# Kernel optimization log

Hardware: AMD Instinct MI355X
Metric: run time of the kernel (lower is better)

## Reference

```python
import jax, jax.numpy as jnp
import numpy as np

CE_WEIGHT = 1.0
TRIPLET_WEIGHT = 0.1
MARGIN = 0.2


def setup_inputs() -> dict:
    key = jax.random.key(0)
    k1, k2, k3 = jax.random.split(key, 3)
    B, D, V = 4096, 512, 6000
    logits = jax.random.normal(k1, (B, V), dtype=jnp.float32)
    embeddings = jax.random.normal(k2, (B, D), dtype=jnp.float32)
    labels = jax.random.randint(k3, (B,), 0, 512, dtype=jnp.int64)
    return {"logits": logits, "embeddings": embeddings, "labels": labels}


def _pairwise_dist(emb):
    # Euclidean cdist via gram matrix; safe sqrt (zero grad where d2 == 0).
    sq = jnp.sum(emb * emb, axis=-1)  # [B]
    d2 = sq[:, None] + sq[None, :] - 2.0 * (emb @ emb.T)  # [B, B]
    d2 = jnp.maximum(d2, 0.0)
    safe = jnp.where(d2 > 0.0, d2, 1.0)
    return jnp.where(d2 > 0.0, jnp.sqrt(safe), 0.0)


def _losses(logits, embeddings, labels):
    B = logits.shape[0]
    # Cross entropy (mean reduction, matching nn.CrossEntropyLoss).
    logp = jax.nn.log_softmax(logits, axis=-1)
    ce_loss = -jnp.mean(jnp.take_along_axis(logp, labels[:, None], axis=1)[:, 0])

    # Batch-hard triplet loss, fully vectorized (one masked amax/amin per row).
    dist = _pairwise_dist(embeddings)  # [B, B]
    same = labels[:, None] == labels[None, :]  # [B, B]
    eye = jnp.eye(B, dtype=bool)
    pos_mask = same & ~eye
    neg_mask = ~same
    neg_inf = jnp.float32(-np.inf)
    pos_inf = jnp.float32(np.inf)
    hardest_pos = jnp.max(jnp.where(pos_mask, dist, neg_inf), axis=1)  # [B]
    hardest_neg = jnp.min(jnp.where(neg_mask, dist, pos_inf), axis=1)  # [B]
    valid = jnp.any(pos_mask, axis=1) & jnp.any(neg_mask, axis=1)  # [B]
    per_row = jax.nn.relu(hardest_pos - hardest_neg + MARGIN)
    per_row = jnp.where(valid, per_row, 0.0)
    n_valid = jnp.sum(valid.astype(jnp.float32))
    triplet_loss = jnp.where(n_valid > 0, jnp.sum(per_row) / jnp.maximum(n_valid, 1.0), 0.0)

    total_loss = CE_WEIGHT * ce_loss + TRIPLET_WEIGHT * triplet_loss
    return total_loss, ce_loss, triplet_loss


def reference(logits, embeddings, labels):
    return _losses(logits, embeddings, labels)
```

## Files before the change

### kernel.cpp

```cpp
#include <hip/hip_runtime.h>
#include <hip/hip_bf16.h>
#include <math.h>

#define BN   4096
#define DN   512
#define VN   6000
#define NCLS 512

typedef __attribute__((ext_vector_type(8)))  short short8;
typedef __attribute__((ext_vector_type(16))) float f32x16;

__device__ __forceinline__ unsigned short f2bf(float x) {
  unsigned int u = __float_as_uint(x);
  u = (u + 0x7FFFu + ((u >> 16) & 1u)) >> 16;
  return (unsigned short)u;
}

__device__ __forceinline__ void gld_lds16(const unsigned short* g, unsigned short* l) {
  __builtin_amdgcn_global_load_lds(
      (const __attribute__((address_space(1))) void*)g,
      (__attribute__((address_space(3))) void*)l, 16, 0, 0);
}

__launch_bounds__(256)
__global__ void prep_kernel(const float* __restrict__ emb, const int* __restrict__ labels,
                            unsigned short* __restrict__ embh, float* __restrict__ sqn,
                            int* __restrict__ cnt, int* __restrict__ posb,
                            int* __restrict__ negb) {
  const int row  = blockIdx.x * 4 + (threadIdx.x >> 6);
  const int lane = threadIdx.x & 63;
  const float4* rp = (const float4*)(emb + (size_t)row * DN);
  float4 a = rp[lane];
  float4 b = rp[lane + 64];
  float ss = a.x * a.x + a.y * a.y + a.z * a.z + a.w * a.w
           + b.x * b.x + b.y * b.y + b.z * b.z + b.w * b.w;
  ushort4 ha, hb;
  ha.x = f2bf(a.x); ha.y = f2bf(a.y); ha.z = f2bf(a.z); ha.w = f2bf(a.w);
  hb.x = f2bf(b.x); hb.y = f2bf(b.y); hb.z = f2bf(b.z); hb.w = f2bf(b.w);
  ushort4* wp = (ushort4*)(embh + (size_t)row * DN);
  wp[lane] = ha;
  wp[lane + 64] = hb;
#pragma unroll
  for (int off = 1; off < 64; off <<= 1) ss += __shfl_xor(ss, off);
  if (lane == 0) {
    sqn[row] = ss;
    posb[row] = 0;
    negb[row] = 0x7F800000;
    atomicAdd(cnt + labels[row], 1);
  }
}

__device__ __forceinline__ void triplet_job(int t, unsigned short* sA, unsigned short* sB,
                                            const unsigned short* __restrict__ embh,
                                            const float* __restrict__ sqn,
                                            const int* __restrict__ labels,
                                            int* __restrict__ posb,
                                            int* __restrict__ negb, int lane) {
  const int m = lane & 31;
  const int half = lane >> 5;

  int J = (int)((sqrtf(8.f * (float)t + 1.f) - 1.f) * 0.5f);
  while ((J + 1) * (J + 2) / 2 <= t) ++J;
  while (J * (J + 1) / 2 > t) --J;
  const int I = t - J * (J + 1) / 2;
  const int i0 = I * 64, j0 = J * 64;
  const bool diag = (I == J);

  const int lrow = lane >> 3;
  const int lchk = (lane & 7) ^ lrow;
  const unsigned short* gA = embh + (size_t)(i0 + lrow) * DN + lchk * 8;
  const unsigned short* gB = embh + (size_t)(j0 + lrow) * DN + lchk * 8;

  f32x16 acc[2][2] = {};
  f32x16 accT[2][2] = {};

  for (int ks = 0; ks < 8; ++ks) {
    const int kk = ks * 64;
    asm volatile("s_waitcnt lgkmcnt(0)" ::: "memory");
#pragma unroll
    for (int s = 0; s < 8; ++s)
      gld_lds16(gA + kk + (size_t)s * 8 * DN, &sA[s * 8 * 64]);
#pragma unroll
    for (int s = 0; s < 8; ++s)
      gld_lds16(gB + kk + (size_t)s * 8 * DN, &sB[s * 8 * 64]);
    asm volatile("s_waitcnt vmcnt(0)" ::: "memory");
#pragma unroll
    for (int q = 0; q < 4; ++q) {
      const int c = q * 2 + half;
      const int sw = ((c ^ (m & 7)) * 8);
      short8 a0 = *(const short8*)&sA[m * 64 + sw];
      short8 a1 = *(const short8*)&sA[(32 + m) * 64 + sw];
      short8 b0 = *(const short8*)&sB[m * 64 + sw];
      short8 b1 = *(const short8*)&sB[(32 + m) * 64 + sw];
      acc[0][0]  = __builtin_amdgcn_mfma_f32_32x32x16_bf16(a0, b0, acc[0][0], 0, 0, 0);
      acc[0][1]  = __builtin_amdgcn_mfma_f32_32x32x16_bf16(a0, b1, acc[0][1], 0, 0, 0);
      acc[1][0]  = __builtin_amdgcn_mfma_f32_32x32x16_bf16(a1, b0, acc[1][0], 0, 0, 0);
      acc[1][1]  = __builtin_amdgcn_mfma_f32_32x32x16_bf16(a1, b1, acc[1][1], 0, 0, 0);
      accT[0][0] = __builtin_amdgcn_mfma_f32_32x32x16_bf16(b0, a0, accT[0][0], 0, 0, 0);
      accT[0][1] = __builtin_amdgcn_mfma_f32_32x32x16_bf16(b0, a1, accT[0][1], 0, 0, 0);
      accT[1][0] = __builtin_amdgcn_mfma_f32_32x32x16_bf16(b1, a0, accT[1][0], 0, 0, 0);
      accT[1][1] = __builtin_amdgcn_mfma_f32_32x32x16_bf16(b1, a1, accT[1][1], 0, 0, 0);
    }
  }

  {
    const int gj0 = j0 + m, gj1 = j0 + 32 + m;
    const int cl0 = labels[gj0], cl1 = labels[gj1];
    const float cq0 = sqn[gj0], cq1 = sqn[gj1];
    float p0 = 0.f, p1 = 0.f, n0 = INFINITY, n1 = INFINITY;
#pragma unroll
    for (int rb = 0; rb < 2; ++rb) {
#pragma unroll
      for (int r = 0; r < 16; ++r) {
        const int gi = i0 + rb * 32 + (r & 3) + 8 * (r >> 2) + 4 * half;
        const int rl = labels[gi];
        const float rq = sqn[gi];
        const float d0 = fmaf(-2.f, acc[rb][0][r], rq + cq0);
        const float d1 = fmaf(-2.f, acc[rb][1][r], rq + cq1);
        if (rl == cl0) { if (gi != gj0) p0 = fmaxf(p0, d0); } else n0 = fminf(n0, d0);
        if (rl == cl1) { if (gi != gj1) p1 = fmaxf(p1, d1); } else n1 = fminf(n1, d1);
      }
    }
    p0 = fmaxf(p0, __shfl_xor(p0, 32)); n0 = fminf(n0, __shfl_xor(n0, 32));
    p1 = fmaxf(p1, __shfl_xor(p1, 32)); n1 = fminf(n1, __shfl_xor(n1, 32));
    if (half == 0) {
      atomicMax(posb + gj0, __float_as_int(p0));
      atomicMin(negb + gj0, __float_as_int(n0));
      atomicMax(posb + gj1, __float_as_int(p1));
      atomicMin(negb + gj1, __float_as_int(n1));
    }
  }

  if (!diag) {
    const int gj0 = i0 + m, gj1 = i0 + 32 + m;
    const int cl0 = labels[gj0], cl1 = labels[gj1];
    const float cq0 = sqn[gj0], cq1 = sqn[gj1];
    float p0 = 0.f, p1 = 0.f, n0 = INFINITY, n1 = INFINITY;
#pragma unroll
    for (int rb = 0; rb < 2; ++rb) {
#pragma unroll
      for (int r = 0; r < 16; ++r) {
        const int gi = j0 + rb * 32 + (r & 3) + 8 * (r >> 2) + 4 * half;
        const int rl = labels[gi];
        const float rq = sqn[gi];
        const float d0 = fmaf(-2.f, accT[rb][0][r], rq + cq0);
        const float d1 = fmaf(-2.f, accT[rb][1][r], rq + cq1);
        if (rl == cl0) p0 = fmaxf(p0, d0); else n0 = fminf(n0, d0);
        if (rl == cl1) p1 = fmaxf(p1, d1); else n1 = fminf(n1, d1);
      }
    }
    p0 = fmaxf(p0, __shfl_xor(p0, 32)); n0 = fminf(n0, __shfl_xor(n0, 32));
    p1 = fmaxf(p1, __shfl_xor(p1, 32)); n1 = fminf(n1, __shfl_xor(n1, 32));
    if (half == 0) {
      atomicMax(posb + gj0, __float_as_int(p0));
      atomicMin(negb + gj0, __float_as_int(n0));
      atomicMax(posb + gj1, __float_as_int(p1));
      atomicMin(negb + gj1, __float_as_int(n1));
    }
  }
}

__launch_bounds__(64, 2)
__global__ void fused_kernel(const float* __restrict__ logits,
                             const int* __restrict__ labels,
                             float* __restrict__ ce_part,
                             const unsigned short* __restrict__ embh,
                             const float* __restrict__ sqn,
                             int* __restrict__ posb, int* __restrict__ negb) {
  __shared__ unsigned short smem[8192];
  const int b = blockIdx.x;
  const int lane = threadIdx.x;

  int trip_job, ce_row;
  if (b < 32) {
    trip_job = 2048 + b; ce_row = -1;
  } else {
    const int g = (b - 32) / 3, r = (b - 32) % 3;
    if (r == 0) { trip_job = g; ce_row = -1; }
    else        { trip_job = -1; ce_row = g * 2 + (r - 1); }
  }

  if (trip_job >= 0) {
    triplet_job(trip_job, smem, smem + 4096, embh, sqn, labels, posb, negb, lane);
    return;
  }

  const float* rp = logits + (size_t)ce_row * VN;
  const float xlab = rp[labels[ce_row]];
  const float4* q = (const float4*)rp;
  float4 v[24];
#pragma unroll
  for (int u = 0; u < 23; ++u) v[u] = q[lane + u * 64];
  if (lane < 28) v[23] = q[lane + 23 * 64];
  float s = 0.f;
#pragma unroll
  for (int u = 0; u < 23; ++u)
    s += __expf(v[u].x) + __expf(v[u].y) + __expf(v[u].z) + __expf(v[u].w);
  if (lane < 28)
    s += __expf(v[23].x) + __expf(v[23].y) + __expf(v[23].z) + __expf(v[23].w);
#pragma unroll
  for (int off = 1; off < 64; off <<= 1) s += __shfl_xor(s, off);
  if (lane == 0) ce_part[ce_row] = logf(s) - xlab;
}

__launch_bounds__(1024)
__global__ void finalize_kernel(const int* __restrict__ posb, const int* __restrict__ negb,
                                const int* __restrict__ labels, const int* __restrict__ cnt,
                                const float* __restrict__ ce_part, float* __restrict__ out) {
  const int tid = threadIdx.x;
  float cesum = 0.f, sum = 0.f, nv = 0.f;
#pragma unroll
  for (int u = 0; u < 4; ++u) {
    const int i = tid + u * 1024;
    cesum += ce_part[i];
    int c = cnt[labels[i]];
    float p = sqrtf(fmaxf(__int_as_float(posb[i]), 0.f));
    float n = sqrtf(fmaxf(__int_as_float(negb[i]), 0.f));
    float t = fmaxf(p - n + 0.2f, 0.f);
    if (c >= 2 && c < BN) { sum += t; nv += 1.f; }
  }
#pragma unroll
  for (int off = 1; off < 64; off <<= 1) {
    cesum += __shfl_xor(cesum, off);
    sum   += __shfl_xor(sum, off);
    nv    += __shfl_xor(nv, off);
  }
  __shared__ float s0[16], s1[16], s2[16];
  if ((tid & 63) == 0) { s0[tid >> 6] = cesum; s1[tid >> 6] = sum; s2[tid >> 6] = nv; }
  __syncthreads();
  if (tid == 0) {
    cesum = 0.f; sum = 0.f; nv = 0.f;
#pragma unroll
    for (int wv = 0; wv < 16; ++wv) { cesum += s0[wv]; sum += s1[wv]; nv += s2[wv]; }
    float trip = (nv > 0.f) ? sum / nv : 0.f;
    float ce = cesum * (1.f / BN);
    out[0] = ce + 0.1f * trip;
    out[1] = ce;
    out[2] = trip;
  }
}

extern "C" void kernel_launch(void* const* d_in, const int* in_sizes, int n_in,
                              void* d_out, int out_size, void* d_ws, size_t ws_size,
                              hipStream_t stream) {
  const float* logits = (const float*)d_in[0];
  const float* emb    = (const float*)d_in[1];
  const int*   labels = (const int*)d_in[2];
  float* out = (float*)d_out;

  char* ws = (char*)d_ws;
  unsigned short* embh = (unsigned short*)ws;
  float* sqn    = (float*)(ws + (size_t)BN * DN * 2);
  int*   posb   = (int*)((char*)sqn  + (size_t)BN * 4);
  int*   negb   = (int*)((char*)posb + (size_t)BN * 4);
  int*   cnt    = (int*)((char*)negb + (size_t)BN * 4);
  float* ce_part = (float*)((char*)cnt + (size_t)NCLS * 4);

  hipMemsetAsync(cnt, 0, (size_t)NCLS * 4, stream);
  hipLaunchKernelGGL(prep_kernel, dim3(BN / 4), dim3(256), 0, stream,
                     emb, labels, embh, sqn, cnt, posb, negb);
  hipLaunchKernelGGL(fused_kernel, dim3(32 + 2048 * 3), dim3(64), 0, stream,
                     logits, labels, ce_part, embh, sqn, posb, negb);
  hipLaunchKernelGGL(finalize_kernel, dim3(1), dim3(1024), 0, stream,
                     posb, negb, labels, cnt, ce_part, out);
}
```

Before: 182.0 us.

## Split fused triplet/CE kernel into separate triplet and cross-entropy kernels

Replaces the single interleaved kernel, which mixed triplet GEMM jobs with per-row cross-entropy blocks, with two sequential launches: a triplet kernel of 2080 single-wave blocks and a CE kernel that processes four rows per 256-thread block. This removes the per-block job dispatch and lets each kernel get its own occupancy and launch bounds. In exchange it gives up overlapping the memory-bound CE reduction with the compute-bound triplet work and adds one extra launch.

```diff
diff --git a/kernel.cpp b/kernel.cpp
--- a/kernel.cpp
+++ b/kernel.cpp
@@ -161,32 +161,23 @@
 }
 
 __launch_bounds__(64, 2)
-__global__ void fused_kernel(const float* __restrict__ logits,
-                             const int* __restrict__ labels,
-                             float* __restrict__ ce_part,
-                             const unsigned short* __restrict__ embh,
-                             const float* __restrict__ sqn,
-                             int* __restrict__ posb, int* __restrict__ negb) {
+__global__ void trip_kernel(const unsigned short* __restrict__ embh,
+                            const float* __restrict__ sqn,
+                            const int* __restrict__ labels,
+                            int* __restrict__ posb, int* __restrict__ negb) {
   __shared__ unsigned short smem[8192];
-  const int b = blockIdx.x;
-  const int lane = threadIdx.x;
-
-  int trip_job, ce_row;
-  if (b < 32) {
-    trip_job = 2048 + b; ce_row = -1;
-  } else {
-    const int g = (b - 32) / 3, r = (b - 32) % 3;
-    if (r == 0) { trip_job = g; ce_row = -1; }
-    else        { trip_job = -1; ce_row = g * 2 + (r - 1); }
-  }
-
-  if (trip_job >= 0) {
-    triplet_job(trip_job, smem, smem + 4096, embh, sqn, labels, posb, negb, lane);
-    return;
-  }
-
-  const float* rp = logits + (size_t)ce_row * VN;
-  const float xlab = rp[labels[ce_row]];
+  triplet_job(blockIdx.x, smem, smem + 4096, embh, sqn, labels, posb, negb,
+              threadIdx.x);
+}
+
+__launch_bounds__(256, 4)
+__global__ void ce_kernel(const float* __restrict__ logits,
+                          const int* __restrict__ labels,
+                          float* __restrict__ ce_part) {
+  const int row  = blockIdx.x * 4 + (threadIdx.x >> 6);
+  const int lane = threadIdx.x & 63;
+  const float* rp = logits + (size_t)row * VN;
+  const float xlab = rp[labels[row]];
   const float4* q = (const float4*)rp;
   float4 v[24];
 #pragma unroll
@@ -200,7 +191,7 @@
     s += __expf(v[23].x) + __expf(v[23].y) + __expf(v[23].z) + __expf(v[23].w);
 #pragma unroll
   for (int off = 1; off < 64; off <<= 1) s += __shfl_xor(s, off);
-  if (lane == 0) ce_part[ce_row] = logf(s) - xlab;
+  if (lane == 0) ce_part[row] = logf(s) - xlab;
 }
 
 __launch_bounds__(1024)
@@ -259,8 +250,10 @@
   hipMemsetAsync(cnt, 0, (size_t)NCLS * 4, stream);
   hipLaunchKernelGGL(prep_kernel, dim3(BN / 4), dim3(256), 0, stream,
                      emb, labels, embh, sqn, cnt, posb, negb);
-  hipLaunchKernelGGL(fused_kernel, dim3(32 + 2048 * 3), dim3(64), 0, stream,
-                     logits, labels, ce_part, embh, sqn, posb, negb);
+  hipLaunchKernelGGL(trip_kernel, dim3(2080), dim3(64), 0, stream,
+                     embh, sqn, labels, posb, negb);
+  hipLaunchKernelGGL(ce_kernel, dim3(BN / 4), dim3(256), 0, stream,
+                     logits, labels, ce_part);
   hipLaunchKernelGGL(finalize_kernel, dim3(1), dim3(1024), 0, stream,
                      posb, negb, labels, cnt, ce_part, out);
 }
```

Measured after the change: 191.7 us. 5.4% more time.

## Drop transposed MFMA accumulators; derive row-side reductions via cross-lane shuffles

Applied to the files above, without the earlier changes.

Off-diagonal tiles of the symmetric Gram matrix used to run a second set of MFMAs (accT) to produce the transposed tile. That set is removed, and the row-side hardest pos/neg values are now reduced from the same acc registers with 5-step butterfly shuffles across the 32 columns, followed by per-row atomics. This halves MFMA work and frees 64 accumulator VGPRs, which is why launch bounds rise to 3 waves per SIMD. In exchange it adds many shuffles and about twice as many atomics per tile.

```diff
diff --git a/kernel.cpp b/kernel.cpp
--- a/kernel.cpp
+++ b/kernel.cpp
@@ -72,7 +72,6 @@
   const unsigned short* gB = embh + (size_t)(j0 + lrow) * DN + lchk * 8;
 
   f32x16 acc[2][2] = {};
-  f32x16 accT[2][2] = {};
 
   for (int ks = 0; ks < 8; ++ks) {
     const int kk = ks * 64;
@@ -92,14 +91,10 @@
       short8 a1 = *(const short8*)&sA[(32 + m) * 64 + sw];
       short8 b0 = *(const short8*)&sB[m * 64 + sw];
       short8 b1 = *(const short8*)&sB[(32 + m) * 64 + sw];
-      acc[0][0]  = __builtin_amdgcn_mfma_f32_32x32x16_bf16(a0, b0, acc[0][0], 0, 0, 0);
-      acc[0][1]  = __builtin_amdgcn_mfma_f32_32x32x16_bf16(a0, b1, acc[0][1], 0, 0, 0);
-      acc[1][0]  = __builtin_amdgcn_mfma_f32_32x32x16_bf16(a1, b0, acc[1][0], 0, 0, 0);
-      acc[1][1]  = __builtin_amdgcn_mfma_f32_32x32x16_bf16(a1, b1, acc[1][1], 0, 0, 0);
-      accT[0][0] = __builtin_amdgcn_mfma_f32_32x32x16_bf16(b0, a0, accT[0][0], 0, 0, 0);
-      accT[0][1] = __builtin_amdgcn_mfma_f32_32x32x16_bf16(b0, a1, accT[0][1], 0, 0, 0);
-      accT[1][0] = __builtin_amdgcn_mfma_f32_32x32x16_bf16(b1, a0, accT[1][0], 0, 0, 0);
-      accT[1][1] = __builtin_amdgcn_mfma_f32_32x32x16_bf16(b1, a1, accT[1][1], 0, 0, 0);
+      acc[0][0] = __builtin_amdgcn_mfma_f32_32x32x16_bf16(a0, b0, acc[0][0], 0, 0, 0);
+      acc[0][1] = __builtin_amdgcn_mfma_f32_32x32x16_bf16(a0, b1, acc[0][1], 0, 0, 0);
+      acc[1][0] = __builtin_amdgcn_mfma_f32_32x32x16_bf16(a1, b0, acc[1][0], 0, 0, 0);
+      acc[1][1] = __builtin_amdgcn_mfma_f32_32x32x16_bf16(a1, b1, acc[1][1], 0, 0, 0);
     }
   }
 
@@ -119,6 +114,20 @@
         const float d1 = fmaf(-2.f, acc[rb][1][r], rq + cq1);
         if (rl == cl0) { if (gi != gj0) p0 = fmaxf(p0, d0); } else n0 = fminf(n0, d0);
         if (rl == cl1) { if (gi != gj1) p1 = fmaxf(p1, d1); } else n1 = fminf(n1, d1);
+        if (!diag) {
+          float pi = 0.f, ni = INFINITY;
+          if (rl == cl0) pi = d0; else ni = d0;
+          if (rl == cl1) pi = fmaxf(pi, d1); else ni = fminf(ni, d1);
+#pragma unroll
+          for (int off = 1; off < 32; off <<= 1) {
+            pi = fmaxf(pi, __shfl_xor(pi, off));
+            ni = fminf(ni, __shfl_xor(ni, off));
+          }
+          if (m == 0) {
+            atomicMax(posb + gi, __float_as_int(pi));
+            atomicMin(negb + gi, __float_as_int(ni));
+          }
+        }
       }
     }
     p0 = fmaxf(p0, __shfl_xor(p0, 32)); n0 = fminf(n0, __shfl_xor(n0, 32));
@@ -130,37 +139,9 @@
       atomicMin(negb + gj1, __float_as_int(n1));
     }
   }
-
-  if (!diag) {
-    const int gj0 = i0 + m, gj1 = i0 + 32 + m;
-    const int cl0 = labels[gj0], cl1 = labels[gj1];
-    const float cq0 = sqn[gj0], cq1 = sqn[gj1];
-    float p0 = 0.f, p1 = 0.f, n0 = INFINITY, n1 = INFINITY;
-#pragma unroll
-    for (int rb = 0; rb < 2; ++rb) {
-#pragma unroll
-      for (int r = 0; r < 16; ++r) {
-        const int gi = j0 + rb * 32 + (r & 3) + 8 * (r >> 2) + 4 * half;
-        const int rl = labels[gi];
-        const float rq = sqn[gi];
-        const float d0 = fmaf(-2.f, accT[rb][0][r], rq + cq0);
-        const float d1 = fmaf(-2.f, accT[rb][1][r], rq + cq1);
-        if (rl == cl0) p0 = fmaxf(p0, d0); else n0 = fminf(n0, d0);
-        if (rl == cl1) p1 = fmaxf(p1, d1); else n1 = fminf(n1, d1);
-      }
-    }
-    p0 = fmaxf(p0, __shfl_xor(p0, 32)); n0 = fminf(n0, __shfl_xor(n0, 32));
-    p1 = fmaxf(p1, __shfl_xor(p1, 32)); n1 = fminf(n1, __shfl_xor(n1, 32));
-    if (half == 0) {
-      atomicMax(posb + gj0, __float_as_int(p0));
-      atomicMin(negb + gj0, __float_as_int(n0));
-      atomicMax(posb + gj1, __float_as_int(p1));
-      atomicMin(negb + gj1, __float_as_int(n1));
-    }
-  }
-}
-
-__launch_bounds__(64, 2)
+}
+
+__launch_bounds__(64, 3)
 __global__ void fused_kernel(const float* __restrict__ logits,
                              const int* __restrict__ labels,
                              float* __restrict__ ce_part,
```

Measured after the change: 194.1 us. 6.7% more time.

## Double-buffer triplet GEMM LDS tiles and stage labels/norms in LDS

Applied to the files above, without the earlier changes.

The triplet tile loop now double-buffers its LDS tiles. The next K-slice is prefetched with global_load_lds while MFMAs run on the current slice, using a partial vmcnt wait in place of a full drain each step. Per-row labels and squared norms are loaded once per lane and staged in shared memory for the epilogue, replacing many scattered global loads. Shared memory per block doubles to 32KB, which may reduce occupancy alongside the other per-block state.

```diff
diff --git a/kernel.cpp b/kernel.cpp
--- a/kernel.cpp
+++ b/kernel.cpp
@@ -50,7 +50,7 @@
   }
 }
 
-__device__ __forceinline__ void triplet_job(int t, unsigned short* sA, unsigned short* sB,
+__device__ __forceinline__ void triplet_job(int t, unsigned short* smem,
                                             const unsigned short* __restrict__ embh,
                                             const float* __restrict__ sqn,
                                             const int* __restrict__ labels,
@@ -66,6 +66,11 @@
   const int i0 = I * 64, j0 = J * 64;
   const bool diag = (I == J);
 
+  const int   li = labels[i0 + lane];
+  const float qi = sqn[i0 + lane];
+  const int   lj = labels[j0 + lane];
+  const float qj = sqn[j0 + lane];
+
   const int lrow = lane >> 3;
   const int lchk = (lane & 7) ^ lrow;
   const unsigned short* gA = embh + (size_t)(i0 + lrow) * DN + lchk * 8;
@@ -74,16 +79,29 @@
   f32x16 acc[2][2] = {};
   f32x16 accT[2][2] = {};
 
+#pragma unroll
+  for (int s = 0; s < 8; ++s) {
+    gld_lds16(gA + (size_t)s * 8 * DN, smem + s * 512);
+    gld_lds16(gB + (size_t)s * 8 * DN, smem + 4096 + s * 512);
+  }
+
   for (int ks = 0; ks < 8; ++ks) {
-    const int kk = ks * 64;
-    asm volatile("s_waitcnt lgkmcnt(0)" ::: "memory");
-#pragma unroll
-    for (int s = 0; s < 8; ++s)
-      gld_lds16(gA + kk + (size_t)s * 8 * DN, &sA[s * 8 * 64]);
-#pragma unroll
-    for (int s = 0; s < 8; ++s)
-      gld_lds16(gB + kk + (size_t)s * 8 * DN, &sB[s * 8 * 64]);
-    asm volatile("s_waitcnt vmcnt(0)" ::: "memory");
+    const int cur = (ks & 1) * 8192;
+    if (ks < 7) {
+      const int nxt = 8192 - cur;
+      const int kk = (ks + 1) * 64;
+      asm volatile("s_waitcnt lgkmcnt(0)" ::: "memory");
+#pragma unroll
+      for (int s = 0; s < 8; ++s) {
+        gld_lds16(gA + kk + (size_t)s * 8 * DN, smem + nxt + s * 512);
+        gld_lds16(gB + kk + (size_t)s * 8 * DN, smem + nxt + 4096 + s * 512);
+      }
+      asm volatile("s_waitcnt vmcnt(16)" ::: "memory");
+    } else {
+      asm volatile("s_waitcnt vmcnt(0)" ::: "memory");
+    }
+    unsigned short* sA = smem + cur;
+    unsigned short* sB = smem + cur + 4096;
 #pragma unroll
     for (int q = 0; q < 4; ++q) {
       const int c = q * 2 + half;
@@ -103,18 +121,25 @@
     }
   }
 
+  int*   sLab = (int*)smem;
+  float* sQn  = (float*)(smem + 256);
+  sLab[lane] = li;  sLab[64 + lane] = lj;
+  sQn[lane]  = qi;  sQn[64 + lane]  = qj;
+  asm volatile("s_waitcnt lgkmcnt(0)" ::: "memory");
+
   {
     const int gj0 = j0 + m, gj1 = j0 + 32 + m;
-    const int cl0 = labels[gj0], cl1 = labels[gj1];
-    const float cq0 = sqn[gj0], cq1 = sqn[gj1];
+    const int cl0 = sLab[64 + m], cl1 = sLab[64 + 32 + m];
+    const float cq0 = sQn[64 + m], cq1 = sQn[64 + 32 + m];
     float p0 = 0.f, p1 = 0.f, n0 = INFINITY, n1 = INFINITY;
 #pragma unroll
     for (int rb = 0; rb < 2; ++rb) {
 #pragma unroll
       for (int r = 0; r < 16; ++r) {
-        const int gi = i0 + rb * 32 + (r & 3) + 8 * (r >> 2) + 4 * half;
-        const int rl = labels[gi];
-        const float rq = sqn[gi];
+        const int ri = rb * 32 + (r & 3) + 8 * (r >> 2) + 4 * half;
+        const int gi = i0 + ri;
+        const int rl = sLab[ri];
+        const float rq = sQn[ri];
         const float d0 = fmaf(-2.f, acc[rb][0][r], rq + cq0);
         const float d1 = fmaf(-2.f, acc[rb][1][r], rq + cq1);
         if (rl == cl0) { if (gi != gj0) p0 = fmaxf(p0, d0); } else n0 = fminf(n0, d0);
@@ -133,16 +158,16 @@
 
   if (!diag) {
     const int gj0 = i0 + m, gj1 = i0 + 32 + m;
-    const int cl0 = labels[gj0], cl1 = labels[gj1];
-    const float cq0 = sqn[gj0], cq1 = sqn[gj1];
+    const int cl0 = sLab[m], cl1 = sLab[32 + m];
+    const float cq0 = sQn[m], cq1 = sQn[32 + m];
     float p0 = 0.f, p1 = 0.f, n0 = INFINITY, n1 = INFINITY;
 #pragma unroll
     for (int rb = 0; rb < 2; ++rb) {
 #pragma unroll
       for (int r = 0; r < 16; ++r) {
-        const int gi = j0 + rb * 32 + (r & 3) + 8 * (r >> 2) + 4 * half;
-        const int rl = labels[gi];
-        const float rq = sqn[gi];
+        const int rj = rb * 32 + (r & 3) + 8 * (r >> 2) + 4 * half;
+        const int rl = sLab[64 + rj];
+        const float rq = sQn[64 + rj];
         const float d0 = fmaf(-2.f, accT[rb][0][r], rq + cq0);
         const float d1 = fmaf(-2.f, accT[rb][1][r], rq + cq1);
         if (rl == cl0) p0 = fmaxf(p0, d0); else n0 = fminf(n0, d0);
@@ -167,7 +192,7 @@
                              const unsigned short* __restrict__ embh,
                              const float* __restrict__ sqn,
                              int* __restrict__ posb, int* __restrict__ negb) {
-  __shared__ unsigned short smem[8192];
+  __shared__ unsigned short smem[16384];
   const int b = blockIdx.x;
   const int lane = threadIdx.x;
 
@@ -181,7 +206,7 @@
   }
 
   if (trip_job >= 0) {
-    triplet_job(trip_job, smem, smem + 4096, embh, sqn, labels, posb, negb, lane);
+    triplet_job(trip_job, smem, embh, sqn, labels, posb, negb, lane);
     return;
   }
 
```

New measurement: 179.2 us. No clear change (-1.5%).
